# Kernel tuning notes

Hardware: AMD Instinct MI355X
Metric: run time of the kernel (lower is better)

Reference implementation:

```python
import jax, jax.numpy as jnp
import numpy as np

HEADS = 8
DIM_HEAD = 64
DIM = 512


def _rotate_half(t):
    # split last dim into two halves, return cat(-x2, x1)  (GPT-NeoX style)
    x1, x2 = jnp.split(t, 2, axis=-1)
    return jnp.concatenate([-x2, x1], axis=-1)


def _apply_rotary(pos, t):
    # pos: [n, d] angles, t: [b, h, n, d]
    cos = jnp.cos(pos)[None, None, :, :]
    sin = jnp.sin(pos)[None, None, :, :]
    return t * cos + _rotate_half(t) * sin


def setup_inputs() -> dict:
    key = jax.random.key(0)
    k1, k2, k3, k4, k5 = jax.random.split(key, 5)
    b, n = 4, 2048
    inner = HEADS * DIM_HEAD
    x = jax.random.normal(k1, (b, n, DIM), dtype=jnp.float32)
    mask = jnp.ones((b, n), dtype=bool)
    rotary_pos = jax.random.uniform(k2, (n, DIM_HEAD), dtype=jnp.float32)
    W_qkv = jax.random.normal(k3, (DIM, inner * 3), dtype=jnp.float32) / np.sqrt(DIM)
    W_out = jax.random.normal(k4, (inner, DIM), dtype=jnp.float32) / np.sqrt(inner)
    b_out = jax.random.normal(k5, (DIM,), dtype=jnp.float32) * 0.01
    return {"x": x, "mask": mask, "rotary_pos": rotary_pos,
            "W_qkv": W_qkv, "W_out": W_out, "b_out": b_out}


def reference(x, mask, rotary_pos, W_qkv, W_out, b_out):
    b, n, _ = x.shape
    h, d = HEADS, DIM_HEAD
    scale = d ** -0.5
    qkv = x @ W_qkv                                  # [b, n, 3*h*d]
    q, k, v = jnp.split(qkv, 3, axis=-1)
    split_heads = lambda t: t.reshape(b, n, h, d).transpose(0, 2, 1, 3)  # b h n d
    q, k, v = map(split_heads, (q, k, v))
    q = _apply_rotary(rotary_pos, q)
    k = _apply_rotary(rotary_pos, k)
    dots = jnp.einsum('bhid,bhjd->bhij', q, k) * scale
    neg = -jnp.finfo(dots.dtype).max
    dots = jnp.where(mask[:, None, None, :], dots, neg)
    attn = jax.nn.softmax(dots, axis=-1)
    out = jnp.einsum('bhij,bhjd->bhid', attn, v)
    out = out.transpose(0, 2, 1, 3).reshape(b, n, h * d)
    return out @ W_out + b_out
```

## Files before the change

kernel.cpp:

```cpp
#include <hip/hip_runtime.h>
#include <hip/hip_bf16.h>
#include <math.h>


#define HEADS 8
#define DHEAD 64
#define DIMM 512
#define BB 4
#define NN 2048
#define QKV_COLS 1536
#define QSCALE 0.18033688011112042f

typedef __attribute__((ext_vector_type(8))) short short8;
typedef __attribute__((ext_vector_type(4))) float floatx4;

static __device__ inline short f2bf(float x) {
    union { float f; unsigned u; } c{x};
    unsigned r = (c.u + 0x7FFF + ((c.u >> 16) & 1)) >> 16;
    return (short)r;
}
static __device__ inline float bf2f(short x) {
    union { unsigned u; float f; } c;
    c.u = ((unsigned)(unsigned short)x) << 16;
    return c.f;
}
static __device__ inline float fast_exp2(float x) {
#if __has_builtin(__builtin_amdgcn_exp2f)
    return __builtin_amdgcn_exp2f(x);
#else
    return exp2f(x);
#endif
}
static __device__ inline unsigned pk2bf(float a, float b) {
    __hip_bfloat162 h = __float22bfloat162_rn(make_float2(a, b));
    union { __hip_bfloat162 h; unsigned u; } c{h};
    return c.u;
}

__global__ __launch_bounds__(256)
void cast_f32_bf16(const float* __restrict__ in, short* __restrict__ out, int n8) {
    int i = blockIdx.x * 256 + threadIdx.x;
    if (i >= n8) return;
    const float4 a = ((const float4*)in)[2 * i];
    const float4 b = ((const float4*)in)[2 * i + 1];
    short8 o;
    o[0] = f2bf(a.x); o[1] = f2bf(a.y); o[2] = f2bf(a.z); o[3] = f2bf(a.w);
    o[4] = f2bf(b.x); o[5] = f2bf(b.y); o[6] = f2bf(b.z); o[7] = f2bf(b.w);
    *(short8*)&out[8 * i] = o;
}

__global__ __launch_bounds__(256)
void transpose_cast(const float* __restrict__ in, short* __restrict__ out,
                    int K, int N) {
    __shared__ short l[32][33];
    const int n0 = blockIdx.x * 32, k0 = blockIdx.y * 32;
    const int c = threadIdx.x & 31, r0 = threadIdx.x >> 5;
    for (int rr = r0; rr < 32; rr += 8)
        l[rr][c] = f2bf(in[(size_t)(k0 + rr) * N + n0 + c]);
    __syncthreads();
    for (int rr = r0; rr < 32; rr += 8)
        out[(size_t)(n0 + rr) * K + k0 + c] = l[c][rr];
}

template<bool BF16_OUT>
__global__ __launch_bounds__(256)
void gemm_bf16(const short* __restrict__ A, const short* __restrict__ Bt,
               const float* __restrict__ bias, void* __restrict__ Cv,
               int M, int N, int K) {
    __shared__ short a_s[128][40];
    __shared__ short b_s[128][40];
    const int t = threadIdx.x;
    const int lane = t & 63, w = t >> 6;
    const int g = lane >> 4, ln = lane & 15;
    const int wr = w >> 1, wc = w & 1;
    const int m0 = blockIdx.y * 128, n0 = blockIdx.x * 128;
    const int srow = t >> 1, sc0 = (t & 1) * 16;

    floatx4 acc[4][4];
#pragma unroll
    for (int i = 0; i < 4; i++)
#pragma unroll
        for (int j = 0; j < 4; j++) acc[i][j] = (floatx4){0.f, 0.f, 0.f, 0.f};

    for (int k0 = 0; k0 < K; k0 += 32) {
        short8 a0 = *(const short8*)&A[(size_t)(m0 + srow) * K + k0 + sc0];
        short8 a1 = *(const short8*)&A[(size_t)(m0 + srow) * K + k0 + sc0 + 8];
        short8 b0 = *(const short8*)&Bt[(size_t)(n0 + srow) * K + k0 + sc0];
        short8 b1 = *(const short8*)&Bt[(size_t)(n0 + srow) * K + k0 + sc0 + 8];
        __syncthreads();
        *(short8*)&a_s[srow][sc0]     = a0;
        *(short8*)&a_s[srow][sc0 + 8] = a1;
        *(short8*)&b_s[srow][sc0]     = b0;
        *(short8*)&b_s[srow][sc0 + 8] = b1;
        __syncthreads();

        short8 af[4], bf_[4];
#pragma unroll
        for (int tm = 0; tm < 4; tm++)
            af[tm] = *(const short8*)&a_s[64 * wr + 16 * tm + ln][g * 8];
#pragma unroll
        for (int tn = 0; tn < 4; tn++)
            bf_[tn] = *(const short8*)&b_s[64 * wc + 16 * tn + ln][g * 8];
#pragma unroll
        for (int tm = 0; tm < 4; tm++)
#pragma unroll
            for (int tn = 0; tn < 4; tn++)
                acc[tm][tn] = __builtin_amdgcn_mfma_f32_16x16x32_bf16(
                    af[tm], bf_[tn], acc[tm][tn], 0, 0, 0);
    }

    float bx[4];
#pragma unroll
    for (int tn = 0; tn < 4; tn++)
        bx[tn] = bias ? bias[n0 + 64 * wc + 16 * tn + ln] : 0.f;

#pragma unroll
    for (int tm = 0; tm < 4; tm++)
#pragma unroll
        for (int r = 0; r < 4; r++) {
            size_t row = (size_t)(m0 + 64 * wr + 16 * tm + g * 4 + r);
#pragma unroll
            for (int tn = 0; tn < 4; tn++) {
                float v = acc[tm][tn][r] + bx[tn];
                size_t col = n0 + 64 * wc + 16 * tn + ln;
                if (BF16_OUT) ((short*)Cv)[row * N + col] = f2bf(v);
                else          ((float*)Cv)[row * N + col] = v;
            }
        }
}

__global__ __launch_bounds__(256)
void pack_rotary(const short* __restrict__ qkv, const float* __restrict__ pos,
                 short* __restrict__ Qb, short* __restrict__ Kb,
                 short* __restrict__ Vt) {
    __shared__ short vt_l[64][68];
    const int t  = threadIdx.x;
    const int n0 = blockIdx.x * 64;
    const int h  = blockIdx.y;
    const int b  = blockIdx.z;
    const short* base = qkv + ((size_t)(b * NN + n0)) * QKV_COLS + h * DHEAD;
    const size_t bh = (size_t)(b * HEADS + h);
    short* qo = Qb + bh * (NN * DHEAD) + (size_t)n0 * DHEAD;
    short* ko = Kb + bh * (NN * DHEAD) + (size_t)n0 * DHEAD;

    for (int f = t; f < 2048; f += 256) {
        int r = f >> 5, dd = f & 31;
        int n = n0 + r;
        float p1 = pos[n * DHEAD + dd], p2 = pos[n * DHEAD + dd + 32];
        float s1, c1, s2, c2;
        __sincosf(p1, &s1, &c1);
        __sincosf(p2, &s2, &c2);
        const short* qp = base + (size_t)r * QKV_COLS;
        float qa = bf2f(qp[dd]), qb = bf2f(qp[dd + 32]);
        qo[r * DHEAD + dd]      = f2bf((qa * c1 - qb * s1) * QSCALE);
        qo[r * DHEAD + dd + 32] = f2bf((qb * c2 + qa * s2) * QSCALE);
        const short* kp = qp + DIMM;
        float ka = bf2f(kp[dd]), kb = bf2f(kp[dd + 32]);
        ko[r * DHEAD + dd]      = f2bf(ka * c1 - kb * s1);
        ko[r * DHEAD + dd + 32] = f2bf(kb * c2 + ka * s2);
        const short* vp = qp + 2 * DIMM;
        int pr = 4 * (r & 15) + (r >> 4);
        vt_l[dd][pr]      = vp[dd];
        vt_l[dd + 32][pr] = vp[dd + 32];
    }
    __syncthreads();
    short* vo = Vt + bh * (size_t)(DHEAD * NN) + n0;
    for (int f = t; f < 512; f += 256) {
        int d = f >> 3, c = (f & 7) * 8;
        *(short8*)&vo[(size_t)d * NN + c] = *(short8*)&vt_l[d][c];
    }
}

__global__ __launch_bounds__(256)
void flash_mfma(const short* __restrict__ Qb, const short* __restrict__ Kb,
                const short* __restrict__ Vt, short* __restrict__ out) {
    __shared__ short k_s[64][68];
    __shared__ short vt_s[64][68];
    __shared__ short p_s[128][68];

    const int t    = threadIdx.x;
    const int lane = t & 63;
    const int w    = t >> 6;
    const int g    = lane >> 4;
    const int ln   = lane & 15;
    const int i0   = blockIdx.x * 128;
    const size_t bh = (size_t)blockIdx.z * HEADS + blockIdx.y;

    const short* Qp = Qb + bh * (NN * DHEAD);
    const short* Kp = Kb + bh * (NN * DHEAD);
    const short* Vp = Vt + bh * (NN * DHEAD);

    short8 qa[2][2];
#pragma unroll
    for (int s = 0; s < 2; s++) {
        const short* qrow = Qp + (size_t)(i0 + 16 * (w + 4 * s) + ln) * DHEAD + g * 8;
        qa[s][0] = *(const short8*)(qrow);
        qa[s][1] = *(const short8*)(qrow + 32);
    }

    floatx4 Oacc[2][4];
#pragma unroll
    for (int s = 0; s < 2; s++)
#pragma unroll
        for (int tn = 0; tn < 4; tn++) Oacc[s][tn] = (floatx4){0.f, 0.f, 0.f, 0.f};
    float lsum[2][4] = {{0.f, 0.f, 0.f, 0.f}, {0.f, 0.f, 0.f, 0.f}};

    const int sr = t >> 2, sc = (t & 3) * 16;

    for (int j0 = 0; j0 < NN; j0 += 64) {
        short8 k0 = *(const short8*)&Kp[(size_t)(j0 + sr) * DHEAD + sc];
        short8 k1 = *(const short8*)&Kp[(size_t)(j0 + sr) * DHEAD + sc + 8];
        short8 v0 = *(const short8*)&Vp[(size_t)sr * NN + j0 + sc];
        short8 v1 = *(const short8*)&Vp[(size_t)sr * NN + j0 + sc + 8];
        __syncthreads();
        *(short8*)&k_s[sr][sc]      = k0;
        *(short8*)&k_s[sr][sc + 8]  = k1;
        *(short8*)&vt_s[sr][sc]     = v0;
        *(short8*)&vt_s[sr][sc + 8] = v1;
        __syncthreads();

        floatx4 sacc[2][4];
#pragma unroll
        for (int tn = 0; tn < 4; tn++) {
            short8 b0 = *(const short8*)&k_s[tn * 16 + ln][g * 8];
            short8 b1 = *(const short8*)&k_s[tn * 16 + ln][g * 8 + 32];
#pragma unroll
            for (int s = 0; s < 2; s++) {
                floatx4 acc = (floatx4){0.f, 0.f, 0.f, 0.f};
                acc = __builtin_amdgcn_mfma_f32_16x16x32_bf16(qa[s][0], b0, acc, 0, 0, 0);
                acc = __builtin_amdgcn_mfma_f32_16x16x32_bf16(qa[s][1], b1, acc, 0, 0, 0);
                sacc[s][tn] = acc;
            }
        }

#pragma unroll
        for (int s = 0; s < 2; s++) {
            int prow0 = 16 * (w + 4 * s) + g * 4;
#pragma unroll
            for (int r = 0; r < 4; r++) {
                float p0 = fast_exp2(sacc[s][0][r]);
                float p1 = fast_exp2(sacc[s][1][r]);
                float p2 = fast_exp2(sacc[s][2][r]);
                float p3 = fast_exp2(sacc[s][3][r]);
                lsum[s][r] += (p0 + p1) + (p2 + p3);
                unsigned u01 = pk2bf(p0, p1);
                unsigned u23 = pk2bf(p2, p3);
                *(uint2*)&p_s[prow0 + r][4 * ln] = make_uint2(u01, u23);
            }
        }

        short8 pa[2][2];
#pragma unroll
        for (int s = 0; s < 2; s++) {
            pa[s][0] = *(const short8*)&p_s[16 * (w + 4 * s) + ln][g * 8];
            pa[s][1] = *(const short8*)&p_s[16 * (w + 4 * s) + ln][g * 8 + 32];
        }
#pragma unroll
        for (int tn = 0; tn < 4; tn++) {
            short8 b0 = *(const short8*)&vt_s[tn * 16 + ln][g * 8];
            short8 b1 = *(const short8*)&vt_s[tn * 16 + ln][g * 8 + 32];
#pragma unroll
            for (int s = 0; s < 2; s++) {
                Oacc[s][tn] = __builtin_amdgcn_mfma_f32_16x16x32_bf16(
                    pa[s][0], b0, Oacc[s][tn], 0, 0, 0);
                Oacc[s][tn] = __builtin_amdgcn_mfma_f32_16x16x32_bf16(
                    pa[s][1], b1, Oacc[s][tn], 0, 0, 0);
            }
        }
    }

#pragma unroll
    for (int s = 0; s < 2; s++) {
        float inv[4];
#pragma unroll
        for (int r = 0; r < 4; r++) {
            float sum = lsum[s][r];
            sum += __shfl_xor(sum, 1, 64);
            sum += __shfl_xor(sum, 2, 64);
            sum += __shfl_xor(sum, 4, 64);
            sum += __shfl_xor(sum, 8, 64);
            inv[r] = 1.f / sum;
        }
        short* ob = out + ((size_t)blockIdx.z * NN + i0 + 16 * (w + 4 * s)) * DIMM
                        + (size_t)blockIdx.y * DHEAD;
#pragma unroll
        for (int tn = 0; tn < 4; tn++)
#pragma unroll
            for (int r = 0; r < 4; r++)
                ob[(size_t)(g * 4 + r) * DIMM + tn * 16 + ln] =
                    f2bf(Oacc[s][tn][r] * inv[r]);
    }
}

extern "C" void kernel_launch(void* const* d_in, const int* in_sizes, int n_in,
                              void* d_out, int out_size, void* d_ws, size_t ws_size,
                              hipStream_t stream) {
    const float* x     = (const float*)d_in[0];
    const float* pos   = (const float*)d_in[2];
    const float* W_qkv = (const float*)d_in[3];
    const float* W_out = (const float*)d_in[4];
    const float* b_out = (const float*)d_in[5];
    float* out = (float*)d_out;

    char* ws = (char*)d_ws;
    short* qkvb = (short*)ws;
    short* attb = (short*)ws;
    short* xb   = (short*)(ws + 25165824);
    short* Qb   = (short*)(ws + 33554432);
    short* Kb   = Qb + (size_t)BB * HEADS * NN * DHEAD;
    short* Vt   = Kb + (size_t)BB * HEADS * NN * DHEAD;
    short* Wqt  = (short*)(ws + 58720256);
    short* Wot  = Wqt + (size_t)QKV_COLS * DIMM;

    cast_f32_bf16<<<(8192 * 512 / 8 + 255) / 256, 256, 0, stream>>>(
        x, xb, 8192 * 512 / 8);
    transpose_cast<<<dim3(QKV_COLS / 32, DIMM / 32), 256, 0, stream>>>(
        W_qkv, Wqt, DIMM, QKV_COLS);
    transpose_cast<<<dim3(DIMM / 32, DIMM / 32), 256, 0, stream>>>(
        W_out, Wot, DIMM, DIMM);
    gemm_bf16<true><<<dim3(QKV_COLS / 128, 8192 / 128), 256, 0, stream>>>(
        xb, Wqt, nullptr, qkvb, 8192, QKV_COLS, DIMM);
    pack_rotary<<<dim3(NN / 64, HEADS, BB), 256, 0, stream>>>(qkvb, pos, Qb, Kb, Vt);
    flash_mfma<<<dim3(NN / 128, HEADS, BB), 256, 0, stream>>>(Qb, Kb, Vt, attb);
    gemm_bf16<false><<<dim3(DIMM / 128, 8192 / 128), 256, 0, stream>>>(
        attb, Wot, b_out, out, 8192, DIMM, DIMM);
}
```

Before: 184.9 us.

## Fuse x cast into QKV GEMM, register-prefetch tiles in GEMM and flash attention

Removes the separate f32-to-bf16 cast kernel for x by having the QKV GEMM load f32 rows and convert them while staging to shared memory. Both the GEMM and flash attention kernels now prefetch the next K-tile into registers while computing the current one, so global latency overlaps with the MFMA work. Flash attention also grows its per-iteration K/V tile to 128 keys, halving the barrier count, and splits work into two 64-key halves with double-buffered P and V shared memory. In exchange, register pressure rises and the shared-memory footprint grows, which may lower occupancy. The wrapped prefetch index also issues one redundant load on the final iteration.

```diff
diff --git a/kernel.cpp b/kernel.cpp
--- a/kernel.cpp
+++ b/kernel.cpp
@@ -35,18 +35,6 @@
     __hip_bfloat162 h = __float22bfloat162_rn(make_float2(a, b));
     union { __hip_bfloat162 h; unsigned u; } c{h};
     return c.u;
-}
-
-__global__ __launch_bounds__(256)
-void cast_f32_bf16(const float* __restrict__ in, short* __restrict__ out, int n8) {
-    int i = blockIdx.x * 256 + threadIdx.x;
-    if (i >= n8) return;
-    const float4 a = ((const float4*)in)[2 * i];
-    const float4 b = ((const float4*)in)[2 * i + 1];
-    short8 o;
-    o[0] = f2bf(a.x); o[1] = f2bf(a.y); o[2] = f2bf(a.z); o[3] = f2bf(a.w);
-    o[4] = f2bf(b.x); o[5] = f2bf(b.y); o[6] = f2bf(b.z); o[7] = f2bf(b.w);
-    *(short8*)&out[8 * i] = o;
 }
 
 __global__ __launch_bounds__(256)
@@ -62,9 +50,9 @@
         out[(size_t)(n0 + rr) * K + k0 + c] = l[c][rr];
 }
 
-template<bool BF16_OUT>
+template<bool BF16_OUT, bool A_F32>
 __global__ __launch_bounds__(256)
-void gemm_bf16(const short* __restrict__ A, const short* __restrict__ Bt,
+void gemm_bf16(const void* __restrict__ Av, const short* __restrict__ Bt,
                const float* __restrict__ bias, void* __restrict__ Cv,
                int M, int N, int K) {
     __shared__ short a_s[128][40];
@@ -82,31 +70,71 @@
 #pragma unroll
         for (int j = 0; j < 4; j++) acc[i][j] = (floatx4){0.f, 0.f, 0.f, 0.f};
 
+    short8 a0, a1, b0, b1;
+    float4 af[4];
+    const short* As = (const short*)Av;
+    const float* Af = (const float*)Av;
+
+    if (A_F32) {
+        const float* p = &Af[(size_t)(m0 + srow) * K + sc0];
+        af[0] = ((const float4*)p)[0]; af[1] = ((const float4*)p)[1];
+        af[2] = ((const float4*)p)[2]; af[3] = ((const float4*)p)[3];
+    } else {
+        a0 = *(const short8*)&As[(size_t)(m0 + srow) * K + sc0];
+        a1 = *(const short8*)&As[(size_t)(m0 + srow) * K + sc0 + 8];
+    }
+    b0 = *(const short8*)&Bt[(size_t)(n0 + srow) * K + sc0];
+    b1 = *(const short8*)&Bt[(size_t)(n0 + srow) * K + sc0 + 8];
+
     for (int k0 = 0; k0 < K; k0 += 32) {
-        short8 a0 = *(const short8*)&A[(size_t)(m0 + srow) * K + k0 + sc0];
-        short8 a1 = *(const short8*)&A[(size_t)(m0 + srow) * K + k0 + sc0 + 8];
-        short8 b0 = *(const short8*)&Bt[(size_t)(n0 + srow) * K + k0 + sc0];
-        short8 b1 = *(const short8*)&Bt[(size_t)(n0 + srow) * K + k0 + sc0 + 8];
         __syncthreads();
-        *(short8*)&a_s[srow][sc0]     = a0;
-        *(short8*)&a_s[srow][sc0 + 8] = a1;
+        if (A_F32) {
+            short8 c0, c1;
+            c0[0] = f2bf(af[0].x); c0[1] = f2bf(af[0].y);
+            c0[2] = f2bf(af[0].z); c0[3] = f2bf(af[0].w);
+            c0[4] = f2bf(af[1].x); c0[5] = f2bf(af[1].y);
+            c0[6] = f2bf(af[1].z); c0[7] = f2bf(af[1].w);
+            c1[0] = f2bf(af[2].x); c1[1] = f2bf(af[2].y);
+            c1[2] = f2bf(af[2].z); c1[3] = f2bf(af[2].w);
+            c1[4] = f2bf(af[3].x); c1[5] = f2bf(af[3].y);
+            c1[6] = f2bf(af[3].z); c1[7] = f2bf(af[3].w);
+            *(short8*)&a_s[srow][sc0]     = c0;
+            *(short8*)&a_s[srow][sc0 + 8] = c1;
+        } else {
+            *(short8*)&a_s[srow][sc0]     = a0;
+            *(short8*)&a_s[srow][sc0 + 8] = a1;
+        }
         *(short8*)&b_s[srow][sc0]     = b0;
         *(short8*)&b_s[srow][sc0 + 8] = b1;
         __syncthreads();
 
-        short8 af[4], bf_[4];
+        {
+            int kn = (k0 + 32) & (K - 1);
+            if (A_F32) {
+                const float* p = &Af[(size_t)(m0 + srow) * K + kn + sc0];
+                af[0] = ((const float4*)p)[0]; af[1] = ((const float4*)p)[1];
+                af[2] = ((const float4*)p)[2]; af[3] = ((const float4*)p)[3];
+            } else {
+                a0 = *(const short8*)&As[(size_t)(m0 + srow) * K + kn + sc0];
+                a1 = *(const short8*)&As[(size_t)(m0 + srow) * K + kn + sc0 + 8];
+            }
+            b0 = *(const short8*)&Bt[(size_t)(n0 + srow) * K + kn + sc0];
+            b1 = *(const short8*)&Bt[(size_t)(n0 + srow) * K + kn + sc0 + 8];
+        }
+
+        short8 aw[4], bw[4];
 #pragma unroll
         for (int tm = 0; tm < 4; tm++)
-            af[tm] = *(const short8*)&a_s[64 * wr + 16 * tm + ln][g * 8];
+            aw[tm] = *(const short8*)&a_s[64 * wr + 16 * tm + ln][g * 8];
 #pragma unroll
         for (int tn = 0; tn < 4; tn++)
-            bf_[tn] = *(const short8*)&b_s[64 * wc + 16 * tn + ln][g * 8];
+            bw[tn] = *(const short8*)&b_s[64 * wc + 16 * tn + ln][g * 8];
 #pragma unroll
         for (int tm = 0; tm < 4; tm++)
 #pragma unroll
             for (int tn = 0; tn < 4; tn++)
                 acc[tm][tn] = __builtin_amdgcn_mfma_f32_16x16x32_bf16(
-                    af[tm], bf_[tn], acc[tm][tn], 0, 0, 0);
+                    aw[tm], bw[tn], acc[tm][tn], 0, 0, 0);
     }
 
     float bx[4];
@@ -174,9 +202,9 @@
 __global__ __launch_bounds__(256)
 void flash_mfma(const short* __restrict__ Qb, const short* __restrict__ Kb,
                 const short* __restrict__ Vt, short* __restrict__ out) {
-    __shared__ short k_s[64][68];
-    __shared__ short vt_s[64][68];
-    __shared__ short p_s[128][68];
+    __shared__ short k_s[128][68];
+    __shared__ short vt_s[2][64][68];
+    __shared__ short p_s[2][128][68];
 
     const int t    = threadIdx.x;
     const int lane = t & 63;
@@ -205,66 +233,84 @@
         for (int tn = 0; tn < 4; tn++) Oacc[s][tn] = (floatx4){0.f, 0.f, 0.f, 0.f};
     float lsum[2][4] = {{0.f, 0.f, 0.f, 0.f}, {0.f, 0.f, 0.f, 0.f}};
 
-    const int sr = t >> 2, sc = (t & 3) * 16;
-
-    for (int j0 = 0; j0 < NN; j0 += 64) {
-        short8 k0 = *(const short8*)&Kp[(size_t)(j0 + sr) * DHEAD + sc];
-        short8 k1 = *(const short8*)&Kp[(size_t)(j0 + sr) * DHEAD + sc + 8];
-        short8 v0 = *(const short8*)&Vp[(size_t)sr * NN + j0 + sc];
-        short8 v1 = *(const short8*)&Vp[(size_t)sr * NN + j0 + sc + 8];
+    const int kr = t >> 1, kc = (t & 1) * 32;
+    const int vd = t >> 2, vh = (t >> 1) & 1, vc = (t & 1) * 32;
+    const int vgc = (t & 3) * 32;
+
+    short8 kp_[4], vp_[4];
+#pragma unroll
+    for (int q = 0; q < 4; q++) {
+        kp_[q] = *(const short8*)&Kp[(size_t)kr * DHEAD + kc + 8 * q];
+        vp_[q] = *(const short8*)&Vp[(size_t)vd * NN + vgc + 8 * q];
+    }
+
+    for (int j0 = 0; j0 < NN; j0 += 128) {
         __syncthreads();
-        *(short8*)&k_s[sr][sc]      = k0;
-        *(short8*)&k_s[sr][sc + 8]  = k1;
-        *(short8*)&vt_s[sr][sc]     = v0;
-        *(short8*)&vt_s[sr][sc + 8] = v1;
+#pragma unroll
+        for (int q = 0; q < 4; q++) {
+            *(short8*)&k_s[kr][kc + 8 * q]      = kp_[q];
+            *(short8*)&vt_s[vh][vd][vc + 8 * q] = vp_[q];
+        }
         __syncthreads();
 
-        floatx4 sacc[2][4];
-#pragma unroll
-        for (int tn = 0; tn < 4; tn++) {
-            short8 b0 = *(const short8*)&k_s[tn * 16 + ln][g * 8];
-            short8 b1 = *(const short8*)&k_s[tn * 16 + ln][g * 8 + 32];
+        {
+            int jn = (j0 + 128) & (NN - 1);
+#pragma unroll
+            for (int q = 0; q < 4; q++) {
+                kp_[q] = *(const short8*)&Kp[(size_t)(jn + kr) * DHEAD + kc + 8 * q];
+                vp_[q] = *(const short8*)&Vp[(size_t)vd * NN + jn + vgc + 8 * q];
+            }
+        }
+
+#pragma unroll
+        for (int h = 0; h < 2; h++) {
+            floatx4 sacc[2][4];
+#pragma unroll
+            for (int tn = 0; tn < 4; tn++) {
+                short8 b0 = *(const short8*)&k_s[h * 64 + tn * 16 + ln][g * 8];
+                short8 b1 = *(const short8*)&k_s[h * 64 + tn * 16 + ln][g * 8 + 32];
+#pragma unroll
+                for (int s = 0; s < 2; s++) {
+                    floatx4 acc = (floatx4){0.f, 0.f, 0.f, 0.f};
+                    acc = __builtin_amdgcn_mfma_f32_16x16x32_bf16(qa[s][0], b0, acc, 0, 0, 0);
+                    acc = __builtin_amdgcn_mfma_f32_16x16x32_bf16(qa[s][1], b1, acc, 0, 0, 0);
+                    sacc[s][tn] = acc;
+                }
+            }
+
 #pragma unroll
             for (int s = 0; s < 2; s++) {
-                floatx4 acc = (floatx4){0.f, 0.f, 0.f, 0.f};
-                acc = __builtin_amdgcn_mfma_f32_16x16x32_bf16(qa[s][0], b0, acc, 0, 0, 0);
-                acc = __builtin_amdgcn_mfma_f32_16x16x32_bf16(qa[s][1], b1, acc, 0, 0, 0);
-                sacc[s][tn] = acc;
-            }
-        }
-
-#pragma unroll
-        for (int s = 0; s < 2; s++) {
-            int prow0 = 16 * (w + 4 * s) + g * 4;
-#pragma unroll
-            for (int r = 0; r < 4; r++) {
-                float p0 = fast_exp2(sacc[s][0][r]);
-                float p1 = fast_exp2(sacc[s][1][r]);
-                float p2 = fast_exp2(sacc[s][2][r]);
-                float p3 = fast_exp2(sacc[s][3][r]);
-                lsum[s][r] += (p0 + p1) + (p2 + p3);
-                unsigned u01 = pk2bf(p0, p1);
-                unsigned u23 = pk2bf(p2, p3);
-                *(uint2*)&p_s[prow0 + r][4 * ln] = make_uint2(u01, u23);
-            }
-        }
-
-        short8 pa[2][2];
-#pragma unroll
-        for (int s = 0; s < 2; s++) {
-            pa[s][0] = *(const short8*)&p_s[16 * (w + 4 * s) + ln][g * 8];
-            pa[s][1] = *(const short8*)&p_s[16 * (w + 4 * s) + ln][g * 8 + 32];
-        }
-#pragma unroll
-        for (int tn = 0; tn < 4; tn++) {
-            short8 b0 = *(const short8*)&vt_s[tn * 16 + ln][g * 8];
-            short8 b1 = *(const short8*)&vt_s[tn * 16 + ln][g * 8 + 32];
+                int prow0 = 16 * (w + 4 * s) + g * 4;
+#pragma unroll
+                for (int r = 0; r < 4; r++) {
+                    float p0 = fast_exp2(sacc[s][0][r]);
+                    float p1 = fast_exp2(sacc[s][1][r]);
+                    float p2 = fast_exp2(sacc[s][2][r]);
+                    float p3 = fast_exp2(sacc[s][3][r]);
+                    lsum[s][r] += (p0 + p1) + (p2 + p3);
+                    unsigned u01 = pk2bf(p0, p1);
+                    unsigned u23 = pk2bf(p2, p3);
+                    *(uint2*)&p_s[h][prow0 + r][4 * ln] = make_uint2(u01, u23);
+                }
+            }
+
+            short8 pa[2][2];
 #pragma unroll
             for (int s = 0; s < 2; s++) {
-                Oacc[s][tn] = __builtin_amdgcn_mfma_f32_16x16x32_bf16(
-                    pa[s][0], b0, Oacc[s][tn], 0, 0, 0);
-                Oacc[s][tn] = __builtin_amdgcn_mfma_f32_16x16x32_bf16(
-                    pa[s][1], b1, Oacc[s][tn], 0, 0, 0);
+                pa[s][0] = *(const short8*)&p_s[h][16 * (w + 4 * s) + ln][g * 8];
+                pa[s][1] = *(const short8*)&p_s[h][16 * (w + 4 * s) + ln][g * 8 + 32];
+            }
+#pragma unroll
+            for (int tn = 0; tn < 4; tn++) {
+                short8 b0 = *(const short8*)&vt_s[h][tn * 16 + ln][g * 8];
+                short8 b1 = *(const short8*)&vt_s[h][tn * 16 + ln][g * 8 + 32];
+#pragma unroll
+                for (int s = 0; s < 2; s++) {
+                    Oacc[s][tn] = __builtin_amdgcn_mfma_f32_16x16x32_bf16(
+                        pa[s][0], b0, Oacc[s][tn], 0, 0, 0);
+                    Oacc[s][tn] = __builtin_amdgcn_mfma_f32_16x16x32_bf16(
+                        pa[s][1], b1, Oacc[s][tn], 0, 0, 0);
+                }
             }
         }
     }
@@ -305,23 +351,20 @@
     char* ws = (char*)d_ws;
     short* qkvb = (short*)ws;
     short* attb = (short*)ws;
-    short* xb   = (short*)(ws + 25165824);
     short* Qb   = (short*)(ws + 33554432);
     short* Kb   = Qb + (size_t)BB * HEADS * NN * DHEAD;
     short* Vt   = Kb + (size_t)BB * HEADS * NN * DHEAD;
     short* Wqt  = (short*)(ws + 58720256);
     short* Wot  = Wqt + (size_t)QKV_COLS * DIMM;
 
-    cast_f32_bf16<<<(8192 * 512 / 8 + 255) / 256, 256, 0, stream>>>(
-        x, xb, 8192 * 512 / 8);
     transpose_cast<<<dim3(QKV_COLS / 32, DIMM / 32), 256, 0, stream>>>(
         W_qkv, Wqt, DIMM, QKV_COLS);
     transpose_cast<<<dim3(DIMM / 32, DIMM / 32), 256, 0, stream>>>(
         W_out, Wot, DIMM, DIMM);
-    gemm_bf16<true><<<dim3(QKV_COLS / 128, 8192 / 128), 256, 0, stream>>>(
-        xb, Wqt, nullptr, qkvb, 8192, QKV_COLS, DIMM);
+    gemm_bf16<true, true><<<dim3(QKV_COLS / 128, 8192 / 128), 256, 0, stream>>>(
+        x, Wqt, nullptr, qkvb, 8192, QKV_COLS, DIMM);
     pack_rotary<<<dim3(NN / 64, HEADS, BB), 256, 0, stream>>>(qkvb, pos, Qb, Kb, Vt);
     flash_mfma<<<dim3(NN / 128, HEADS, BB), 256, 0, stream>>>(Qb, Kb, Vt, attb);
-    gemm_bf16<false><<<dim3(DIMM / 128, 8192 / 128), 256, 0, stream>>>(
+    gemm_bf16<false, false><<<dim3(DIMM / 128, 8192 / 128), 256, 0, stream>>>(
         attb, Wot, b_out, out, 8192, DIMM, DIMM);
 }
```

New measurement: 187.9 us. Within noise of the previous version (+1.6%).

## Split flash attention KV loop across two thread groups with register prefetch

Applied to the files above, without the earlier changes.

The flash attention kernel now launches 512 threads per block, split into two 256-thread groups. Each group processes alternate 64-key tiles with its own LDS buffers, and the partial O accumulators and row sums are merged through LDS at the end. The next K/V tile is also prefetched into registers while the current tile is computed. The aim is more waves per block to hide latency, in exchange for more registers per block, a final reduction step, and a softmax that is not max-subtracted, so the split only stays correct because of that.

```diff
diff --git a/kernel.cpp b/kernel.cpp
--- a/kernel.cpp
+++ b/kernel.cpp
@@ -171,21 +171,24 @@
     }
 }
 
-__global__ __launch_bounds__(256)
+__global__ __launch_bounds__(512)
 void flash_mfma(const short* __restrict__ Qb, const short* __restrict__ Kb,
                 const short* __restrict__ Vt, short* __restrict__ out) {
-    __shared__ short k_s[64][68];
-    __shared__ short vt_s[64][68];
-    __shared__ short p_s[128][68];
-
+    __shared__ short lds[34816];
     const int t    = threadIdx.x;
-    const int lane = t & 63;
-    const int w    = t >> 6;
+    const int grp  = t >> 8;
+    const int tl   = t & 255;
+    const int lane = tl & 63;
+    const int w    = tl >> 6;
     const int g    = lane >> 4;
     const int ln   = lane & 15;
     const int i0   = blockIdx.x * 128;
     const size_t bh = (size_t)blockIdx.z * HEADS + blockIdx.y;
 
+    short (*k_s)[68]  = (short(*)[68])(lds + grp * 4352);
+    short (*vt_s)[68] = (short(*)[68])(lds + 8704 + grp * 4352);
+    short (*p_s)[68]  = (short(*)[68])(lds + 17408 + grp * 8704);
+
     const short* Qp = Qb + bh * (NN * DHEAD);
     const short* Kp = Kb + bh * (NN * DHEAD);
     const short* Vp = Vt + bh * (NN * DHEAD);
@@ -205,19 +208,29 @@
         for (int tn = 0; tn < 4; tn++) Oacc[s][tn] = (floatx4){0.f, 0.f, 0.f, 0.f};
     float lsum[2][4] = {{0.f, 0.f, 0.f, 0.f}, {0.f, 0.f, 0.f, 0.f}};
 
-    const int sr = t >> 2, sc = (t & 3) * 16;
-
-    for (int j0 = 0; j0 < NN; j0 += 64) {
-        short8 k0 = *(const short8*)&Kp[(size_t)(j0 + sr) * DHEAD + sc];
-        short8 k1 = *(const short8*)&Kp[(size_t)(j0 + sr) * DHEAD + sc + 8];
-        short8 v0 = *(const short8*)&Vp[(size_t)sr * NN + j0 + sc];
-        short8 v1 = *(const short8*)&Vp[(size_t)sr * NN + j0 + sc + 8];
+    const int sr = tl >> 2, sc = (tl & 3) * 16;
+    const int jg = 64 * grp;
+
+    short8 k0 = *(const short8*)&Kp[(size_t)(jg + sr) * DHEAD + sc];
+    short8 k1 = *(const short8*)&Kp[(size_t)(jg + sr) * DHEAD + sc + 8];
+    short8 v0 = *(const short8*)&Vp[(size_t)sr * NN + jg + sc];
+    short8 v1 = *(const short8*)&Vp[(size_t)sr * NN + jg + sc + 8];
+
+    for (int it = 0; it < NN / 128; it++) {
         __syncthreads();
         *(short8*)&k_s[sr][sc]      = k0;
         *(short8*)&k_s[sr][sc + 8]  = k1;
         *(short8*)&vt_s[sr][sc]     = v0;
         *(short8*)&vt_s[sr][sc + 8] = v1;
         __syncthreads();
+
+        {
+            int jn = (128 * it + 128 + jg) & (NN - 1);
+            k0 = *(const short8*)&Kp[(size_t)(jn + sr) * DHEAD + sc];
+            k1 = *(const short8*)&Kp[(size_t)(jn + sr) * DHEAD + sc + 8];
+            v0 = *(const short8*)&Vp[(size_t)sr * NN + jn + sc];
+            v1 = *(const short8*)&Vp[(size_t)sr * NN + jn + sc + 8];
+        }
 
         floatx4 sacc[2][4];
 #pragma unroll
@@ -269,26 +282,56 @@
         }
     }
 
-#pragma unroll
-    for (int s = 0; s < 2; s++) {
-        float inv[4];
-#pragma unroll
-        for (int r = 0; r < 4; r++) {
-            float sum = lsum[s][r];
-            sum += __shfl_xor(sum, 1, 64);
-            sum += __shfl_xor(sum, 2, 64);
-            sum += __shfl_xor(sum, 4, 64);
-            sum += __shfl_xor(sum, 8, 64);
-            inv[r] = 1.f / sum;
-        }
-        short* ob = out + ((size_t)blockIdx.z * NN + i0 + 16 * (w + 4 * s)) * DIMM
-                        + (size_t)blockIdx.y * DHEAD;
-#pragma unroll
-        for (int tn = 0; tn < 4; tn++)
-#pragma unroll
-            for (int r = 0; r < 4; r++)
-                ob[(size_t)(g * 4 + r) * DIMM + tn * 16 + ln] =
-                    f2bf(Oacc[s][tn][r] * inv[r]);
+    float* scr = (float*)lds;
+    __syncthreads();
+    if (grp == 1) {
+        float* p = scr + tl * 41;
+#pragma unroll
+        for (int s = 0; s < 2; s++)
+#pragma unroll
+            for (int tn = 0; tn < 4; tn++)
+                *(floatx4*)&p[(s * 4 + tn) * 4] = Oacc[s][tn];
+#pragma unroll
+        for (int s = 0; s < 2; s++)
+#pragma unroll
+            for (int r = 0; r < 4; r++) p[32 + s * 4 + r] = lsum[s][r];
+    }
+    __syncthreads();
+    if (grp == 0) {
+        float* p = scr + tl * 41;
+#pragma unroll
+        for (int s = 0; s < 2; s++)
+#pragma unroll
+            for (int tn = 0; tn < 4; tn++) {
+                floatx4 o = *(floatx4*)&p[(s * 4 + tn) * 4];
+                Oacc[s][tn] += o;
+            }
+#pragma unroll
+        for (int s = 0; s < 2; s++)
+#pragma unroll
+            for (int r = 0; r < 4; r++) lsum[s][r] += p[32 + s * 4 + r];
+
+#pragma unroll
+        for (int s = 0; s < 2; s++) {
+            float inv[4];
+#pragma unroll
+            for (int r = 0; r < 4; r++) {
+                float sum = lsum[s][r];
+                sum += __shfl_xor(sum, 1, 64);
+                sum += __shfl_xor(sum, 2, 64);
+                sum += __shfl_xor(sum, 4, 64);
+                sum += __shfl_xor(sum, 8, 64);
+                inv[r] = 1.f / sum;
+            }
+            short* ob = out + ((size_t)blockIdx.z * NN + i0 + 16 * (w + 4 * s)) * DIMM
+                            + (size_t)blockIdx.y * DHEAD;
+#pragma unroll
+            for (int tn = 0; tn < 4; tn++)
+#pragma unroll
+                for (int r = 0; r < 4; r++)
+                    ob[(size_t)(g * 4 + r) * DIMM + tn * 16 + ln] =
+                        f2bf(Oacc[s][tn][r] * inv[r]);
+        }
     }
 }
 
@@ -321,7 +364,7 @@
     gemm_bf16<true><<<dim3(QKV_COLS / 128, 8192 / 128), 256, 0, stream>>>(
         xb, Wqt, nullptr, qkvb, 8192, QKV_COLS, DIMM);
     pack_rotary<<<dim3(NN / 64, HEADS, BB), 256, 0, stream>>>(qkvb, pos, Qb, Kb, Vt);
-    flash_mfma<<<dim3(NN / 128, HEADS, BB), 256, 0, stream>>>(Qb, Kb, Vt, attb);
+    flash_mfma<<<dim3(NN / 128, HEADS, BB), 512, 0, stream>>>(Qb, Kb, Vt, attb);
     gemm_bf16<false><<<dim3(DIMM / 128, 8192 / 128), 256, 0, stream>>>(
         attb, Wot, b_out, out, 8192, DIMM, DIMM);
 }
```

Result: slower. 313.1 us (+69.3%).
